# Optimization experiments

Measured on AMD Instinct MI355X. Metric: run time of the kernel, lower is better.

The kernel has to match this reference:

```python
import jax, jax.numpy as jnp
import numpy as np

EMBED_DIM = 1024
BATCH, SEQ = 4, 2048


def setup_inputs() -> dict:
    key = jax.random.key(0)
    k1, k2 = jax.random.split(key)
    hidden_states = jax.random.normal(k1, (BATCH, SEQ, EMBED_DIM), dtype=jnp.float32)
    # fused QKV projection weight (Linear(embed_dim, 3*embed_dim, bias=False)),
    # stored as [E, 3E] so y = x @ W
    W_qkv = jax.random.normal(k2, (EMBED_DIM, 3 * EMBED_DIM), dtype=jnp.float32) * (1.0 / np.sqrt(EMBED_DIM))
    return {"hidden_states": hidden_states, "W_qkv": W_qkv}


def reference(hidden_states, W_qkv):
    E = hidden_states.shape[-1]
    scale = 1.0 / np.sqrt(E)
    qkv = jnp.einsum('bse,ef->bsf', hidden_states, W_qkv)  # [B,S,3E]
    q, k, v = jnp.split(qkv, 3, axis=-1)                   # each [B,S,E]
    # scores = q @ (k^T * scale); softmax over keys
    scores = jnp.einsum('bqe,bke->bqk', q, k) * scale      # [B,S,S]
    w = jax.nn.softmax(scores, axis=-1)
    return jnp.einsum('bqk,bke->bqe', w, v)                # [B,S,E]
```

## Files before the change

### kernel.cpp

```cpp
#include <hip/hip_runtime.h>

typedef __attribute__((ext_vector_type(8))) short short8;
typedef __attribute__((ext_vector_type(8))) unsigned short ushort8;
typedef __attribute__((ext_vector_type(4))) float f32x4;

__device__ __forceinline__ float bf2f(unsigned short u) {
  union { unsigned int u; float f; } c; c.u = ((unsigned int)u) << 16; return c.f;
}
__device__ __forceinline__ unsigned short f2bf(float f) {
  union { float f; unsigned int u; } c; c.f = f;
  unsigned int x = c.u;
  return (unsigned short)((x + 0x7FFFu + ((x >> 16) & 1u)) >> 16);
}

#define GLD_LDS16(g, l)                                                        \
  __builtin_amdgcn_global_load_lds(                                            \
      (const __attribute__((address_space(1))) void*)(g),                      \
      (__attribute__((address_space(3))) void*)(l), 16, 0, 0)

__global__ __launch_bounds__(256) void prep_kernel(
    const float* __restrict__ X, unsigned short* __restrict__ Xb,
    const float* __restrict__ W, unsigned short* __restrict__ Wt,
    float* __restrict__ Lrow) {
  const int t = threadIdx.x;
  if (blockIdx.x < 4096) {
    long i = ((long)blockIdx.x * 256 + t) * 8;
    float4 a = *(const float4*)(X + i);
    float4 b = *(const float4*)(X + i + 4);
    ushort8 o;
    o[0] = f2bf(a.x); o[1] = f2bf(a.y); o[2] = f2bf(a.z); o[3] = f2bf(a.w);
    o[4] = f2bf(b.x); o[5] = f2bf(b.y); o[6] = f2bf(b.z); o[7] = f2bf(b.w);
    *(ushort8*)(Xb + i) = o;
  } else if (blockIdx.x < 4864) {
    const int bid = blockIdx.x - 4096;
    const int f0 = (bid % 48) * 64;
    const int e0 = (bid / 48) * 64;
    __shared__ unsigned short tile[64][65];
    const int cg = (t & 15) * 4;
    const int r = t >> 4;
#pragma unroll
    for (int i = 0; i < 4; ++i) {
      int e = r + i * 16;
      float4 v = *(const float4*)(W + (long)(e0 + e) * 3072 + f0 + cg);
      tile[e][cg + 0] = f2bf(v.x);
      tile[e][cg + 1] = f2bf(v.y);
      tile[e][cg + 2] = f2bf(v.z);
      tile[e][cg + 3] = f2bf(v.w);
    }
    __syncthreads();
#pragma unroll
    for (int i = 0; i < 4; ++i) {
      int f = (t >> 4) + i * 16;
      int e = (t & 15) * 4;
      ushort4 o;
      o.x = tile[e + 0][f];
      o.y = tile[e + 1][f];
      o.z = tile[e + 2][f];
      o.w = tile[e + 3][f];
      *(ushort4*)(Wt + (long)(f0 + f) * 1024 + e0 + e) = o;
    }
  } else {
    float4 z = {0.f, 0.f, 0.f, 0.f};
#pragma unroll
    for (int j = 0; j < 8; ++j) *(float4*)(Lrow + (j * 256 + t) * 4) = z;
  }
}

template <int MODE>
__device__ __forceinline__ void gemm_body(
    const unsigned short* __restrict__ A, const unsigned short* __restrict__ B,
    void* __restrict__ Cv, int K, int lda, int ldb, int ldc,
    long sA, long sB, long sC, float alpha, float* __restrict__ Lrow,
    unsigned short* __restrict__ Vt) {
  constexpr int BM = 128, BN = 128, BK = 64;
  __shared__ __align__(16) unsigned short smem[BM * BK + BN * BK];
  unsigned short* As = smem;
  unsigned short* Bs = smem + BM * BK;

  const int t = threadIdx.x;
  const int lane = t & 63;
  const int wave = t >> 6;
  const int quad = lane >> 4;
  const int mrow = lane & 15;
  const int wm = wave >> 1, wn = wave & 1;

  const int bx = blockIdx.x, by = blockIdx.y;
  const int rowA0 = by * BM;
  const int rowB0 = bx * BN;
  const int b = blockIdx.z;
  const unsigned short* Ab = A + (long)b * sA;
  const unsigned short* Bb = B + (long)b * sB;

  f32x4 acc[4][4];
#pragma unroll
  for (int i = 0; i < 4; ++i)
#pragma unroll
    for (int j = 0; j < 4; ++j) {
      f32x4 z = {0.f, 0.f, 0.f, 0.f};
      acc[i][j] = z;
    }

  const int rbase = wave * 32 + (lane >> 3);
  const int c2 = lane & 7;

  for (int kt = 0; kt < K; kt += BK) {
#pragma unroll
    for (int j = 0; j < 4; ++j) {
      int r = rbase + j * 8;
      int c = c2 ^ (r & 7);
      GLD_LDS16(Ab + (long)(rowA0 + r) * lda + kt + c * 8, As + (wave * 4 + j) * 512);
      GLD_LDS16(Bb + (long)(rowB0 + r) * ldb + kt + c * 8, Bs + (wave * 4 + j) * 512);
    }
    __syncthreads();
#pragma unroll
    for (int ks = 0; ks < 2; ++ks) {
      short8 af[4], bfr[4];
#pragma unroll
      for (int i = 0; i < 4; ++i) {
        int rA = wm * 64 + i * 16 + mrow;
        int cc = ks * 4 + quad;
        af[i] = *(const short8*)(As + (rA * 8 + (cc ^ (rA & 7))) * 8);
        int rB = wn * 64 + i * 16 + mrow;
        bfr[i] = *(const short8*)(Bs + (rB * 8 + (cc ^ (rB & 7))) * 8);
      }
#pragma unroll
      for (int mt = 0; mt < 4; ++mt)
#pragma unroll
        for (int nt = 0; nt < 4; ++nt)
          acc[mt][nt] = __builtin_amdgcn_mfma_f32_16x16x32_bf16(
              af[mt], bfr[nt], acc[mt][nt], 0, 0, 0);
    }
    __syncthreads();
  }

  const int m_base = rowA0 + wm * 64;
  const int n_base = rowB0 + wn * 64;
  const long cb = (long)b * sC;

  if constexpr (MODE == 0) {
    if (bx < 16) {
#pragma unroll
      for (int mt = 0; mt < 4; ++mt)
#pragma unroll
        for (int nt = 0; nt < 4; ++nt)
#pragma unroll
          for (int i = 0; i < 4; ++i) {
            int row = m_base + mt * 16 + quad * 4 + i;
            int col = n_base + nt * 16 + mrow;
            ((unsigned short*)Cv)[cb + (long)row * ldc + col] = f2bf(acc[mt][nt][i]);
          }
    } else {
#pragma unroll
      for (int mt = 0; mt < 4; ++mt)
#pragma unroll
        for (int nt = 0; nt < 4; ++nt) {
          int r4 = wm * 64 + mt * 16 + quad * 4;
          int cL = wn * 64 + nt * 16 + mrow;
          int swz = ((cL & 7) << 4) ^ (((cL >> 3) & 3) << 3);
          ushort4 pk;
          pk.x = f2bf(acc[mt][nt][0]);
          pk.y = f2bf(acc[mt][nt][1]);
          pk.z = f2bf(acc[mt][nt][2]);
          pk.w = f2bf(acc[mt][nt][3]);
          *(ushort4*)(smem + cL * 128 + (r4 ^ swz)) = pk;
        }
      __syncthreads();
      const int batch = by >> 4;
      const int s_base = (by & 15) * 128;
      const int e_base = (bx - 16) * 128;
      unsigned short* VtB = Vt + (long)batch * 1024 * 2048;
#pragma unroll
      for (int rnd = 0; rnd < 8; ++rnd) {
        int e = (t >> 4) + rnd * 16;
        int s = (t & 15) * 8;
        int swz = ((e & 7) << 4) ^ (((e >> 3) & 3) << 3);
        ushort8 v = *(const ushort8*)(smem + e * 128 + (s ^ swz));
        *(ushort8*)(VtB + (long)(e_base + e) * 2048 + s_base + s) = v;
      }
    }
  } else if constexpr (MODE == 1) {
    float p[4][4];
#pragma unroll
    for (int mt = 0; mt < 4; ++mt)
#pragma unroll
      for (int i = 0; i < 4; ++i) p[mt][i] = 0.f;
#pragma unroll
    for (int mt = 0; mt < 4; ++mt)
#pragma unroll
      for (int nt = 0; nt < 4; ++nt)
#pragma unroll
        for (int i = 0; i < 4; ++i) {
          int row = m_base + mt * 16 + quad * 4 + i;
          int col = n_base + nt * 16 + mrow;
          float e = __expf(acc[mt][nt][i] * alpha);
          ((unsigned short*)Cv)[cb + (long)row * ldc + col] = f2bf(e);
          p[mt][i] += e;
        }
#pragma unroll
    for (int off = 1; off < 16; off <<= 1)
#pragma unroll
      for (int mt = 0; mt < 4; ++mt)
#pragma unroll
        for (int i = 0; i < 4; ++i)
          p[mt][i] += __shfl_xor(p[mt][i], off, 64);
    if (mrow == 0) {
#pragma unroll
      for (int mt = 0; mt < 4; ++mt)
#pragma unroll
        for (int i = 0; i < 4; ++i) {
          int row = m_base + mt * 16 + quad * 4 + i;
          atomicAdd(&Lrow[b * 2048 + row], p[mt][i]);
        }
    }
  } else {
#pragma unroll
    for (int mt = 0; mt < 4; ++mt)
#pragma unroll
      for (int i = 0; i < 4; ++i) {
        int row = m_base + mt * 16 + quad * 4 + i;
        float inv = 1.0f / Lrow[b * 2048 + row];
#pragma unroll
        for (int nt = 0; nt < 4; ++nt) {
          int col = n_base + nt * 16 + mrow;
          ((float*)Cv)[cb + (long)row * ldc + col] = acc[mt][nt][i] * inv;
        }
      }
  }
}

__global__ __launch_bounds__(256, 2) void qkv_gemm_kernel(
    const unsigned short* __restrict__ A, const unsigned short* __restrict__ B,
    void* __restrict__ Cv, int K, int lda, int ldb, int ldc,
    long sA, long sB, long sC, float alpha, float* __restrict__ Lrow,
    unsigned short* __restrict__ Vt) {
  gemm_body<0>(A, B, Cv, K, lda, ldb, ldc, sA, sB, sC, alpha, Lrow, Vt);
}
__global__ __launch_bounds__(256, 2) void score_gemm_kernel(
    const unsigned short* __restrict__ A, const unsigned short* __restrict__ B,
    void* __restrict__ Cv, int K, int lda, int ldb, int ldc,
    long sA, long sB, long sC, float alpha, float* __restrict__ Lrow,
    unsigned short* __restrict__ Vt) {
  gemm_body<1>(A, B, Cv, K, lda, ldb, ldc, sA, sB, sC, alpha, Lrow, Vt);
}
__global__ __launch_bounds__(256, 2) void out_gemm_kernel(
    const unsigned short* __restrict__ A, const unsigned short* __restrict__ B,
    void* __restrict__ Cv, int K, int lda, int ldb, int ldc,
    long sA, long sB, long sC, float alpha, float* __restrict__ Lrow,
    unsigned short* __restrict__ Vt) {
  gemm_body<2>(A, B, Cv, K, lda, ldb, ldc, sA, sB, sC, alpha, Lrow, Vt);
}

extern "C" void kernel_launch(void* const* d_in, const int* in_sizes, int n_in,
                              void* d_out, int out_size, void* d_ws, size_t ws_size,
                              hipStream_t stream) {
  const float* X = (const float*)d_in[0];
  const float* W = (const float*)d_in[1];
  float* out = (float*)d_out;

  char* ws = (char*)d_ws;
  unsigned short* Xb  = (unsigned short*)(ws);
  unsigned short* Wtb = (unsigned short*)(ws + 16777216);
  unsigned short* QK  = (unsigned short*)(ws + 23068672);
  unsigned short* Vt  = (unsigned short*)(ws + 56623104);
  unsigned short* Sb  = (unsigned short*)(ws + 73400320);
  float* Lrow         = (float*)(ws + 106954752);

  prep_kernel<<<4865, 256, 0, stream>>>(X, Xb, W, Wtb, Lrow);

  qkv_gemm_kernel<<<dim3(24, 64, 1), 256, 0, stream>>>(
      Xb, Wtb, QK, 1024, 1024, 1024, 2048, 0L, 0L, 0L, 1.0f, nullptr, Vt);

  score_gemm_kernel<<<dim3(16, 16, 4), 256, 0, stream>>>(
      QK, QK + 1024, Sb, 1024, 2048, 2048, 2048,
      (long)2048 * 2048, (long)2048 * 2048, (long)2048 * 2048, 0.03125f, Lrow, nullptr);

  out_gemm_kernel<<<dim3(8, 16, 4), 256, 0, stream>>>(
      Sb, Vt, out, 2048, 2048, 2048, 1024,
      (long)2048 * 2048, (long)1024 * 2048, (long)2048 * 1024, 1.0f, Lrow, nullptr);
}
```

Measured before the change: 227.8 us.

## Add dedicated producer wave with double-buffered LDS in GEMM kernels

The GEMM body now runs with a fifth wave that only issues global-to-LDS loads for the next K tile into a second LDS buffer, while the four original waves run MFMA on the current buffer. This is meant to overlap global memory latency with matrix math instead of the earlier load, barrier, compute, barrier sequence. The epilogues are gated to the compute waves. In exchange, LDS use per block doubles to 64KB, and a single wave must issue every load for a tile, which may itself become a bottleneck.

```diff
diff --git a/kernel.cpp b/kernel.cpp
--- a/kernel.cpp
+++ b/kernel.cpp
@@ -73,16 +73,14 @@
     long sA, long sB, long sC, float alpha, float* __restrict__ Lrow,
     unsigned short* __restrict__ Vt) {
   constexpr int BM = 128, BN = 128, BK = 64;
-  __shared__ __align__(16) unsigned short smem[BM * BK + BN * BK];
-  unsigned short* As = smem;
-  unsigned short* Bs = smem + BM * BK;
+  __shared__ __align__(16) unsigned short smem[2][16384];
 
   const int t = threadIdx.x;
   const int lane = t & 63;
   const int wave = t >> 6;
   const int quad = lane >> 4;
   const int mrow = lane & 15;
-  const int wm = wave >> 1, wn = wave & 1;
+  const int wm = (wave & 3) >> 1, wn = wave & 1;
 
   const int bx = blockIdx.x, by = blockIdx.y;
   const int rowA0 = by * BM;
@@ -100,35 +98,56 @@
       acc[i][j] = z;
     }
 
-  const int rbase = wave * 32 + (lane >> 3);
   const int c2 = lane & 7;
-
-  for (int kt = 0; kt < K; kt += BK) {
-#pragma unroll
-    for (int j = 0; j < 4; ++j) {
-      int r = rbase + j * 8;
+  const int rlane = lane >> 3;
+  const int nT = K / BK;
+
+  if (wave == 4) {
+#pragma unroll
+    for (int j2 = 0; j2 < 16; ++j2) {
+      int r = j2 * 8 + rlane;
       int c = c2 ^ (r & 7);
-      GLD_LDS16(Ab + (long)(rowA0 + r) * lda + kt + c * 8, As + (wave * 4 + j) * 512);
-      GLD_LDS16(Bb + (long)(rowB0 + r) * ldb + kt + c * 8, Bs + (wave * 4 + j) * 512);
-    }
-    __syncthreads();
-#pragma unroll
-    for (int ks = 0; ks < 2; ++ks) {
-      short8 af[4], bfr[4];
-#pragma unroll
-      for (int i = 0; i < 4; ++i) {
-        int rA = wm * 64 + i * 16 + mrow;
-        int cc = ks * 4 + quad;
-        af[i] = *(const short8*)(As + (rA * 8 + (cc ^ (rA & 7))) * 8);
-        int rB = wn * 64 + i * 16 + mrow;
-        bfr[i] = *(const short8*)(Bs + (rB * 8 + (cc ^ (rB & 7))) * 8);
-      }
-#pragma unroll
-      for (int mt = 0; mt < 4; ++mt)
-#pragma unroll
-        for (int nt = 0; nt < 4; ++nt)
-          acc[mt][nt] = __builtin_amdgcn_mfma_f32_16x16x32_bf16(
-              af[mt], bfr[nt], acc[mt][nt], 0, 0, 0);
+      GLD_LDS16(Ab + (long)(rowA0 + r) * lda + c * 8, &smem[0][j2 * 512]);
+      GLD_LDS16(Bb + (long)(rowB0 + r) * ldb + c * 8, &smem[0][8192 + j2 * 512]);
+    }
+  }
+  __syncthreads();
+
+  for (int it = 0; it < nT; ++it) {
+    const unsigned short* As = &smem[it & 1][0];
+    const unsigned short* Bs = &smem[it & 1][8192];
+    if (wave == 4) {
+      if (it + 1 < nT) {
+        const int kt = (it + 1) * BK;
+        unsigned short* nA = &smem[(it + 1) & 1][0];
+        unsigned short* nB = &smem[(it + 1) & 1][8192];
+#pragma unroll
+        for (int j2 = 0; j2 < 16; ++j2) {
+          int r = j2 * 8 + rlane;
+          int c = c2 ^ (r & 7);
+          GLD_LDS16(Ab + (long)(rowA0 + r) * lda + kt + c * 8, nA + j2 * 512);
+          GLD_LDS16(Bb + (long)(rowB0 + r) * ldb + kt + c * 8, nB + j2 * 512);
+        }
+      }
+    } else {
+#pragma unroll
+      for (int ks = 0; ks < 2; ++ks) {
+        short8 af[4], bfr[4];
+#pragma unroll
+        for (int i = 0; i < 4; ++i) {
+          int rA = wm * 64 + i * 16 + mrow;
+          int cc = ks * 4 + quad;
+          af[i] = *(const short8*)(As + (rA * 8 + (cc ^ (rA & 7))) * 8);
+          int rB = wn * 64 + i * 16 + mrow;
+          bfr[i] = *(const short8*)(Bs + (rB * 8 + (cc ^ (rB & 7))) * 8);
+        }
+#pragma unroll
+        for (int mt = 0; mt < 4; ++mt)
+#pragma unroll
+          for (int nt = 0; nt < 4; ++nt)
+            acc[mt][nt] = __builtin_amdgcn_mfma_f32_16x16x32_bf16(
+                af[mt], bfr[nt], acc[mt][nt], 0, 0, 0);
+      }
     }
     __syncthreads();
   }
@@ -139,6 +158,59 @@
 
   if constexpr (MODE == 0) {
     if (bx < 16) {
+      if (wave < 4) {
+#pragma unroll
+        for (int mt = 0; mt < 4; ++mt)
+#pragma unroll
+          for (int nt = 0; nt < 4; ++nt)
+#pragma unroll
+            for (int i = 0; i < 4; ++i) {
+              int row = m_base + mt * 16 + quad * 4 + i;
+              int col = n_base + nt * 16 + mrow;
+              ((unsigned short*)Cv)[cb + (long)row * ldc + col] = f2bf(acc[mt][nt][i]);
+            }
+      }
+    } else {
+      unsigned short* sm = &smem[0][0];
+      if (wave < 4) {
+#pragma unroll
+        for (int mt = 0; mt < 4; ++mt)
+#pragma unroll
+          for (int nt = 0; nt < 4; ++nt) {
+            int r4 = wm * 64 + mt * 16 + quad * 4;
+            int cL = wn * 64 + nt * 16 + mrow;
+            int swz = ((cL & 7) << 4) ^ (((cL >> 3) & 3) << 3);
+            ushort4 pk;
+            pk.x = f2bf(acc[mt][nt][0]);
+            pk.y = f2bf(acc[mt][nt][1]);
+            pk.z = f2bf(acc[mt][nt][2]);
+            pk.w = f2bf(acc[mt][nt][3]);
+            *(ushort4*)(sm + cL * 128 + (r4 ^ swz)) = pk;
+          }
+      }
+      __syncthreads();
+      if (wave < 4) {
+        const int batch = by >> 4;
+        const int s_base = (by & 15) * 128;
+        const int e_base = (bx - 16) * 128;
+        unsigned short* VtB = Vt + (long)batch * 1024 * 2048;
+#pragma unroll
+        for (int rnd = 0; rnd < 8; ++rnd) {
+          int e = (t >> 4) + rnd * 16;
+          int s = (t & 15) * 8;
+          int swz = ((e & 7) << 4) ^ (((e >> 3) & 3) << 3);
+          ushort8 v = *(const ushort8*)(sm + e * 128 + (s ^ swz));
+          *(ushort8*)(VtB + (long)(e_base + e) * 2048 + s_base + s) = v;
+        }
+      }
+    }
+  } else if constexpr (MODE == 1) {
+    if (wave < 4) {
+      float p[4][4];
+#pragma unroll
+      for (int mt = 0; mt < 4; ++mt)
+#pragma unroll
+        for (int i = 0; i < 4; ++i) p[mt][i] = 0.f;
 #pragma unroll
       for (int mt = 0; mt < 4; ++mt)
 #pragma unroll
@@ -147,102 +219,60 @@
           for (int i = 0; i < 4; ++i) {
             int row = m_base + mt * 16 + quad * 4 + i;
             int col = n_base + nt * 16 + mrow;
-            ((unsigned short*)Cv)[cb + (long)row * ldc + col] = f2bf(acc[mt][nt][i]);
+            float e = __expf(acc[mt][nt][i] * alpha);
+            ((unsigned short*)Cv)[cb + (long)row * ldc + col] = f2bf(e);
+            p[mt][i] += e;
           }
-    } else {
+#pragma unroll
+      for (int off = 1; off < 16; off <<= 1)
+#pragma unroll
+        for (int mt = 0; mt < 4; ++mt)
+#pragma unroll
+          for (int i = 0; i < 4; ++i)
+            p[mt][i] += __shfl_xor(p[mt][i], off, 64);
+      if (mrow == 0) {
+#pragma unroll
+        for (int mt = 0; mt < 4; ++mt)
+#pragma unroll
+          for (int i = 0; i < 4; ++i) {
+            int row = m_base + mt * 16 + quad * 4 + i;
+            atomicAdd(&Lrow[b * 2048 + row], p[mt][i]);
+          }
+      }
+    }
+  } else {
+    if (wave < 4) {
 #pragma unroll
       for (int mt = 0; mt < 4; ++mt)
-#pragma unroll
-        for (int nt = 0; nt < 4; ++nt) {
-          int r4 = wm * 64 + mt * 16 + quad * 4;
-          int cL = wn * 64 + nt * 16 + mrow;
-          int swz = ((cL & 7) << 4) ^ (((cL >> 3) & 3) << 3);
-          ushort4 pk;
-          pk.x = f2bf(acc[mt][nt][0]);
-          pk.y = f2bf(acc[mt][nt][1]);
-          pk.z = f2bf(acc[mt][nt][2]);
-          pk.w = f2bf(acc[mt][nt][3]);
-          *(ushort4*)(smem + cL * 128 + (r4 ^ swz)) = pk;
-        }
-      __syncthreads();
-      const int batch = by >> 4;
-      const int s_base = (by & 15) * 128;
-      const int e_base = (bx - 16) * 128;
-      unsigned short* VtB = Vt + (long)batch * 1024 * 2048;
-#pragma unroll
-      for (int rnd = 0; rnd < 8; ++rnd) {
-        int e = (t >> 4) + rnd * 16;
-        int s = (t & 15) * 8;
-        int swz = ((e & 7) << 4) ^ (((e >> 3) & 3) << 3);
-        ushort8 v = *(const ushort8*)(smem + e * 128 + (s ^ swz));
-        *(ushort8*)(VtB + (long)(e_base + e) * 2048 + s_base + s) = v;
-      }
-    }
-  } else if constexpr (MODE == 1) {
-    float p[4][4];
-#pragma unroll
-    for (int mt = 0; mt < 4; ++mt)
-#pragma unroll
-      for (int i = 0; i < 4; ++i) p[mt][i] = 0.f;
-#pragma unroll
-    for (int mt = 0; mt < 4; ++mt)
-#pragma unroll
-      for (int nt = 0; nt < 4; ++nt)
 #pragma unroll
         for (int i = 0; i < 4; ++i) {
           int row = m_base + mt * 16 + quad * 4 + i;
-          int col = n_base + nt * 16 + mrow;
-          float e = __expf(acc[mt][nt][i] * alpha);
-          ((unsigned short*)Cv)[cb + (long)row * ldc + col] = f2bf(e);
-          p[mt][i] += e;
+          float inv = 1.0f / Lrow[b * 2048 + row];
+#pragma unroll
+          for (int nt = 0; nt < 4; ++nt) {
+            int col = n_base + nt * 16 + mrow;
+            ((float*)Cv)[cb + (long)row * ldc + col] = acc[mt][nt][i] * inv;
+          }
         }
-#pragma unroll
-    for (int off = 1; off < 16; off <<= 1)
-#pragma unroll
-      for (int mt = 0; mt < 4; ++mt)
-#pragma unroll
-        for (int i = 0; i < 4; ++i)
-          p[mt][i] += __shfl_xor(p[mt][i], off, 64);
-    if (mrow == 0) {
-#pragma unroll
-      for (int mt = 0; mt < 4; ++mt)
-#pragma unroll
-        for (int i = 0; i < 4; ++i) {
-          int row = m_base + mt * 16 + quad * 4 + i;
-          atomicAdd(&Lrow[b * 2048 + row], p[mt][i]);
-        }
-    }
-  } else {
-#pragma unroll
-    for (int mt = 0; mt < 4; ++mt)
-#pragma unroll
-      for (int i = 0; i < 4; ++i) {
-        int row = m_base + mt * 16 + quad * 4 + i;
-        float inv = 1.0f / Lrow[b * 2048 + row];
-#pragma unroll
-        for (int nt = 0; nt < 4; ++nt) {
-          int col = n_base + nt * 16 + mrow;
-          ((float*)Cv)[cb + (long)row * ldc + col] = acc[mt][nt][i] * inv;
-        }
-      }
+    }
   }
 }
 
-__global__ __launch_bounds__(256, 2) void qkv_gemm_kernel(
+__global__ __launch_bounds__(320, 2) void qkv_gemm_kernel(
     const unsigned short* __restrict__ A, const unsigned short* __restrict__ B,
     void* __restrict__ Cv, int K, int lda, int ldb, int ldc,
     long sA, long sB, long sC, float alpha, float* __restrict__ Lrow,
     unsigned short* __restrict__ Vt) {
   gemm_body<0>(A, B, Cv, K, lda, ldb, ldc, sA, sB, sC, alpha, Lrow, Vt);
 }
-__global__ __launch_bounds__(256, 2) void score_gemm_kernel(
+__global__ __launch_bounds__(320, 2) void score_gemm_kernel(
     const unsigned short* __restrict__ A, const unsigned short* __restrict__ B,
     void* __restrict__ Cv, int K, int lda, int ldb, int ldc,
     long sA, long sB, long sC, float alpha, float* __restrict__ Lrow,
     unsigned short* __restrict__ Vt) {
   gemm_body<1>(A, B, Cv, K, lda, ldb, ldc, sA, sB, sC, alpha, Lrow, Vt);
 }
-__global__ __launch_bounds__(256, 2) void out_gemm_kernel(
+__global__ __launch_bounds__(320, 2) void out_gemm_kernel(
     const unsigned short* __restrict__ A, const unsigned short* __restrict__ B,
     void* __restrict__ Cv, int K, int lda, int ldb, int ldc,
     long sA, long sB, long sC, float alpha, float* __restrict__ Lrow,
@@ -267,14 +297,14 @@
 
   prep_kernel<<<4865, 256, 0, stream>>>(X, Xb, W, Wtb, Lrow);
 
-  qkv_gemm_kernel<<<dim3(24, 64, 1), 256, 0, stream>>>(
+  qkv_gemm_kernel<<<dim3(24, 64, 1), 320, 0, stream>>>(
       Xb, Wtb, QK, 1024, 1024, 1024, 2048, 0L, 0L, 0L, 1.0f, nullptr, Vt);
 
-  score_gemm_kernel<<<dim3(16, 16, 4), 256, 0, stream>>>(
+  score_gemm_kernel<<<dim3(16, 16, 4), 320, 0, stream>>>(
       QK, QK + 1024, Sb, 1024, 2048, 2048, 2048,
       (long)2048 * 2048, (long)2048 * 2048, (long)2048 * 2048, 0.03125f, Lrow, nullptr);
 
-  out_gemm_kernel<<<dim3(8, 16, 4), 256, 0, stream>>>(
+  out_gemm_kernel<<<dim3(8, 16, 4), 320, 0, stream>>>(
       Sb, Vt, out, 2048, 2048, 2048, 1024,
       (long)2048 * 2048, (long)1024 * 2048, (long)2048 * 1024, 1.0f, Lrow, nullptr);
 }
```

Result: slower. 314.1 us (+37.9%).
